# Performance work log

Measured on AMD Instinct MI355X. Metric: run time of the kernel, lower is better.

The kernel has to match this reference:

```python
import jax, jax.numpy as jnp
import numpy as np

EMSIZE = 2048
NCLASS = 128
D1 = 2
D2 = 2
NSENT = 32768


def setup_inputs() -> dict:
    key = jax.random.key(0)
    k1, k2, k3 = jax.random.split(key, 3)
    x = jax.random.normal(k1, (NSENT, 1, EMSIZE), dtype=jnp.float32)
    # Scaled-normal params (original uses nn.init.normal_; scaling keeps tanh unsaturated)
    W1 = jax.random.normal(k2, (D1 + 1, EMSIZE, NCLASS), dtype=jnp.float32) / np.float32(np.sqrt(EMSIZE))
    b1 = jnp.zeros((1, NCLASS), dtype=jnp.float32)
    W2 = jax.random.normal(k3, (D2 + 1, NCLASS, NCLASS), dtype=jnp.float32) / np.float32(np.sqrt(NCLASS))
    b2 = jnp.zeros((1, NCLASS), dtype=jnp.float32)
    return {"structural_representations": x, "W1": W1, "b1": b1, "W2": W2, "b2": b2}


def _shift_down(y, k, n):
    # y[p] -> y[p-k], zeros for p < k (causal shift along sentence axis)
    return jnp.pad(y, ((k, 0), (0, 0)))[:n] if k > 0 else y


def reference(structural_representations, W1, b1, W2, b2):
    x = structural_representations  # [N, 1, E]
    n, _, e = x.shape
    d1 = W1.shape[0] - 1
    d2 = W2.shape[0] - 1
    c = W1.shape[-1]
    xs = x.reshape(n, e)  # [N, E]

    # Stage 1: S[p] = sum_{k=0..d1, k<=p} (x[p-k] @ W1[k] + b1)
    Y = jnp.einsum('ne,kec->knc', xs, W1)  # [d1+1, N, C]: one big GEMM per tap
    S = sum(_shift_down(Y[k], k, n) for k in range(d1 + 1))  # windowed causal sum
    pos = jnp.arange(n)
    cnt1 = (jnp.minimum(pos, d1) + 1).astype(xs.dtype)  # bias added once per valid tap
    H = jnp.tanh(S + cnt1[:, None] * b1[0])  # [N, C]

    # Stage 2 (i >= d2): Z[i] = sum_{j=0..d2} H[i-d2+j] @ W2[j] + (d2+1)*b2
    G = jnp.einsum('nc,kcd->knd', H, W2)  # [d2+1, N, C]
    Z = sum(_shift_down(G[j], d2 - j, n) for j in range(d2 + 1)) + (d2 + 1) * b2[0]

    # Fallback for i < d2: single term tanh(x[i]@W1[0]+b1) @ W2[0] + b2
    H0 = jnp.tanh(xs @ W1[0] + b1[0])
    Z0 = H0 @ W2[0] + b2[0]
    Z = jnp.where((pos >= d2)[:, None], Z, Z0)

    out = jax.nn.log_softmax(Z, axis=-1)
    return out.reshape(n, 1, c)
```

## Files before the change

kernel.cpp:

```cpp
#include <hip/hip_runtime.h>
#include <math.h>

typedef __attribute__((ext_vector_type(8))) short short8;
typedef __attribute__((ext_vector_type(4))) float f32x4;

#define MFMA16(a, b, c) __builtin_amdgcn_mfma_f32_16x16x32_bf16((a), (b), (c), 0, 0, 0)

__device__ inline void gl_lds16(const void* g, void* l) {
  __builtin_amdgcn_global_load_lds(
      (const __attribute__((address_space(1))) void*)g,
      (__attribute__((address_space(3))) void*)l, 16, 0, 0);
}

__device__ inline unsigned int pack2(float lo, float hi) {
  unsigned int ulo = __float_as_uint(lo), uhi = __float_as_uint(hi);
  return (uhi & 0xFFFF0000u) | (ulo >> 16);
}
__device__ inline unsigned short f2bf_r(float f) {
  return (unsigned short)((__float_as_uint(f) + 0x8000u) >> 16);
}
__device__ inline float bf2f(unsigned short h) {
  return __uint_as_float(((unsigned int)h) << 16);
}

__global__ __launch_bounds__(256) void k_repack(const float* __restrict__ W1,
                                                const float* __restrict__ W2,
                                                unsigned short* __restrict__ W1bt,
                                                unsigned short* __restrict__ W2t) {
  __shared__ float tile[64 * 128];
  const int b = blockIdx.x, tid = threadIdx.x;
  if (b < 96) {
    const int k = b >> 5, et = b & 31;
    const int e0 = et * 64;
    const float* src = W1 + (size_t)k * 262144 + (size_t)e0 * 128;
#pragma unroll
    for (int i = 0; i < 8; ++i) {
      int idx4 = tid + i * 256;
      ((f32x4*)tile)[idx4] = ((const f32x4*)src)[idx4];
    }
    __syncthreads();
#pragma unroll
    for (int i = 0; i < 4; ++i) {
      int item = tid + i * 256;
      int c = item >> 3, eo = (item & 7) * 8;
      union { unsigned short h[8]; uint4 v; } t;
#pragma unroll
      for (int u = 0; u < 8; ++u) t.h[u] = f2bf_r(tile[(eo + u) * 128 + c]);
      *(uint4*)(W1bt + (size_t)(k * 128 + c) * 2048 + e0 + eo) = t.v;
    }
  } else {
    int idx = (b - 96) * 256 + tid;
    int j = idx >> 14, r = idx & 16383, d = r >> 7, c = r & 127;
    W2t[idx] = f2bf_r(W2[(size_t)j * 16384 + (size_t)c * 128 + d]);
  }
}

__global__ __launch_bounds__(256, 2) void k_fused(const float* __restrict__ X,
                                                  const unsigned short* __restrict__ Bt,
                                                  const unsigned short* __restrict__ W2t,
                                                  const float* __restrict__ b1,
                                                  const float* __restrict__ b2,
                                                  float* __restrict__ out) {
  __shared__ __align__(16) char smem[66560];
  float* Alds = (float*)smem;
  unsigned short* Blds = (unsigned short*)(smem + 17408);
  unsigned short* Yt = (unsigned short*)smem;
  float* zbuf = (float*)(smem + 62720);

  const int r0 = blockIdx.x * 64;
  const int tid = threadIdx.x, wave = tid >> 6, lane = tid & 63;
  const int mrow = lane & 15, quad = lane >> 4;

  const float* agp[5];
#pragma unroll
  for (int r = 0; r < 4; ++r) {
    int i = wave * 16 + r * 4 + (lane >> 4);
    int g = r0 - 4 + i; if (g < 0) g = 0;
    int c = (lane & 15) ^ (i & 15);
    agp[r] = X + (size_t)g * 2048 + c * 4;
  }
  {
    int i = 64 + (lane >> 4);
    int c = (lane & 15) ^ (i & 15);
    agp[4] = X + (size_t)(r0 - 4 + i) * 2048 + c * 4;
  }
  const unsigned short* bgp[12];
#pragma unroll
  for (int r = 0; r < 12; ++r) {
    int col = wave * 96 + r * 8 + (lane >> 3);
    int c = (lane & 7) ^ (col & 7);
    bgp[r] = Bt + (size_t)col * 2048 + c * 8;
  }

  f32x4 acc[5][6] = {};

  for (int k0 = 0; k0 < 2048; k0 += 64) {
#pragma unroll
    for (int r = 0; r < 4; ++r)
      gl_lds16(agp[r], (char*)Alds + (wave * 16 + r * 4) * 256);
    if (wave == 0) gl_lds16(agp[4], (char*)Alds + 64 * 256);
#pragma unroll
    for (int r = 0; r < 12; ++r)
      gl_lds16(bgp[r], (char*)Blds + (wave * 96 + r * 8) * 128);
#pragma unroll
    for (int r = 0; r < 5; ++r) agp[r] += 64;
#pragma unroll
    for (int r = 0; r < 12; ++r) bgp[r] += 64;
    __syncthreads();

#pragma unroll
    for (int s = 0; s < 2; ++s) {
      short8 af[5];
#pragma unroll
      for (int rt = 0; rt < 5; ++rt) {
        int row = rt * 16 + mrow;
        int c0 = s * 8 + quad * 2;
        const float* base = Alds + row * 64;
        f32x4 x0 = *(const f32x4*)(base + ((c0 ^ mrow) * 4));
        f32x4 x1 = *(const f32x4*)(base + (((c0 + 1) ^ mrow) * 4));
        union { unsigned int u[4]; short8 v; } t;
        t.u[0] = pack2(x0[0], x0[1]); t.u[1] = pack2(x0[2], x0[3]);
        t.u[2] = pack2(x1[0], x1[1]); t.u[3] = pack2(x1[2], x1[3]);
        af[rt] = t.v;
      }
#pragma unroll
      for (int ct = 0; ct < 6; ++ct) {
        int col = wave * 96 + ct * 16 + mrow;
        int ch = (s * 4 + quad) ^ (mrow & 7);
        short8 bf = *(const short8*)(Blds + col * 64 + ch * 8);
#pragma unroll
        for (int rt = 0; rt < 5; ++rt)
          acc[rt][ct] = MFMA16(af[rt], bf, acc[rt][ct]);
      }
    }
    __syncthreads();
  }

#pragma unroll
  for (int rt = 0; rt < 5; ++rt)
#pragma unroll
    for (int ct = 0; ct < 6; ++ct)
#pragma unroll
      for (int rg = 0; rg < 4; ++rg) {
        int l = rt * 16 + quad * 4 + rg;
        int col = wave * 96 + ct * 16 + mrow;
        Yt[l * 392 + col] = f2bf_r(acc[rt][ct][rg]);
      }
  __syncthreads();

  for (int idx = tid; idx < 66 * 128; idx += 256) {
    int hl = idx >> 7, c = idx & 127;
    int p = r0 - 2 + hl;
    int i = hl + 2;
    float h = 0.f;
    if (p >= 0) {
      float s = bf2f(Yt[i * 392 + c]);
      float cnt = 1.f;
      if (p >= 1) { s += bf2f(Yt[(i - 1) * 392 + 128 + c]); cnt += 1.f; }
      if (p >= 2) { s += bf2f(Yt[(i - 2) * 392 + 256 + c]); cnt += 1.f; }
      h = tanhf(fmaf(cnt, b1[c], s));
    }
    Yt[(i - 2) * 392 + 256 + c] = f2bf_r(h);
  }
  __syncthreads();

  f32x4 acc2[8] = {};
#pragma unroll
  for (int j = 0; j < 3; ++j) {
#pragma unroll
    for (int kk = 0; kk < 4; ++kk) {
      short8 a0 = *(const short8*)&Yt[(wave * 16 + mrow + j) * 392 + 256 + kk * 32 + quad * 8];
      const unsigned short* wp = W2t + (size_t)(j * 128 + mrow) * 128 + kk * 32 + quad * 8;
#pragma unroll
      for (int ct = 0; ct < 8; ++ct)
        acc2[ct] = MFMA16(a0, *(const short8*)(wp + ct * 16 * 128), acc2[ct]);
    }
  }

#pragma unroll
  for (int rg = 0; rg < 4; ++rg) {
    float z[8]; float m = -1e30f;
#pragma unroll
    for (int ct = 0; ct < 8; ++ct) {
      z[ct] = acc2[ct][rg] + 3.f * b2[ct * 16 + mrow];
      m = fmaxf(m, z[ct]);
    }
#pragma unroll
    for (int off = 1; off < 16; off <<= 1) m = fmaxf(m, __shfl_xor(m, off, 64));
    float s = 0.f;
#pragma unroll
    for (int ct = 0; ct < 8; ++ct) s += __expf(z[ct] - m);
#pragma unroll
    for (int off = 1; off < 16; off <<= 1) s += __shfl_xor(s, off, 64);
    float lse = m + __logf(s);
    int grow = r0 + wave * 16 + quad * 4 + rg;
    if (grow >= 2) {
      float* op = out + (size_t)grow * 128 + mrow;
#pragma unroll
      for (int ct = 0; ct < 8; ++ct) op[ct * 16] = z[ct] - lse;
    }
  }

  if (blockIdx.x == 0) {
    __syncthreads();
    int row = tid >> 7, d = tid & 127;
    zbuf[row * 128 + d] = tanhf(bf2f(Yt[(row + 4) * 392 + d]) + b1[d]);
    __syncthreads();
    float zv = b2[d];
    for (int c = 0; c < 128; ++c)
      zv = fmaf(zbuf[row * 128 + c], bf2f(W2t[(size_t)d * 128 + c]), zv);
    __syncthreads();
    zbuf[row * 128 + d] = zv;
    __syncthreads();
    float m = -1e30f;
    for (int c = 0; c < 128; ++c) m = fmaxf(m, zbuf[row * 128 + c]);
    float s = 0.f;
    for (int c = 0; c < 128; ++c) s += __expf(zbuf[row * 128 + c] - m);
    out[(size_t)row * 128 + d] = zv - m - __logf(s);
  }
}

extern "C" void kernel_launch(void* const* d_in, const int* in_sizes, int n_in,
                              void* d_out, int out_size, void* d_ws, size_t ws_size,
                              hipStream_t stream) {
  const float* X  = (const float*)d_in[0];
  const float* W1 = (const float*)d_in[1];
  const float* b1 = (const float*)d_in[2];
  const float* W2 = (const float*)d_in[3];
  const float* b2 = (const float*)d_in[4];
  float* out = (float*)d_out;

  unsigned short* W1bt = (unsigned short*)d_ws;
  unsigned short* W2t  = (unsigned short*)((char*)d_ws + 1572864);

  k_repack<<<288, 256, 0, stream>>>(W1, W2, W1bt, W2t);
  k_fused<<<512, 256, 0, stream>>>(X, W1bt, W2t, b1, b2, out);
}
```

Baseline: 424.0 us.

## Double-buffer LDS tiles in fused GEMM main loop, one block per CU

Doubles the shared-memory allocation so the next K-tile of X and W1 can be loaded asynchronously into one buffer while MFMAs read the other. The per-iteration barrier before compute goes away and only the end-of-loop barrier remains. The aim is to hide global-load latency inside each block. In exchange, launch bounds drop to one block per CU, so the 512 blocks now run in two waves and inter-block latency hiding is lost.

```diff
diff --git a/kernel.cpp b/kernel.cpp
--- a/kernel.cpp
+++ b/kernel.cpp
@@ -55,15 +55,13 @@
   }
 }
 
-__global__ __launch_bounds__(256, 2) void k_fused(const float* __restrict__ X,
+__global__ __launch_bounds__(256, 1) void k_fused(const float* __restrict__ X,
                                                   const unsigned short* __restrict__ Bt,
                                                   const unsigned short* __restrict__ W2t,
                                                   const float* __restrict__ b1,
                                                   const float* __restrict__ b2,
                                                   float* __restrict__ out) {
-  __shared__ __align__(16) char smem[66560];
-  float* Alds = (float*)smem;
-  unsigned short* Blds = (unsigned short*)(smem + 17408);
+  __shared__ __align__(16) char smem[133120];
   unsigned short* Yt = (unsigned short*)smem;
   float* zbuf = (float*)(smem + 62720);
 
@@ -94,20 +92,32 @@
 
   f32x4 acc[5][6] = {};
 
-  for (int k0 = 0; k0 < 2048; k0 += 64) {
+  auto stage = [&](char* base) {
+    char* An = base;
+    char* Bn = base + 17408;
 #pragma unroll
     for (int r = 0; r < 4; ++r)
-      gl_lds16(agp[r], (char*)Alds + (wave * 16 + r * 4) * 256);
-    if (wave == 0) gl_lds16(agp[4], (char*)Alds + 64 * 256);
+      gl_lds16(agp[r], An + (wave * 16 + r * 4) * 256);
+    if (wave == 0) gl_lds16(agp[4], An + 64 * 256);
 #pragma unroll
     for (int r = 0; r < 12; ++r)
-      gl_lds16(bgp[r], (char*)Blds + (wave * 96 + r * 8) * 128);
+      gl_lds16(bgp[r], Bn + (wave * 96 + r * 8) * 128);
 #pragma unroll
     for (int r = 0; r < 5; ++r) agp[r] += 64;
 #pragma unroll
     for (int r = 0; r < 12; ++r) bgp[r] += 64;
-    __syncthreads();
-
+  };
+
+  stage(smem);
+  __syncthreads();
+
+#pragma unroll 2
+  for (int t = 0; t < 32; ++t) {
+    const int cur = t & 1;
+    if (t < 31) stage(smem + (cur ^ 1) * 66560);
+
+    const float* Af = (const float*)(smem + cur * 66560);
+    const unsigned short* Bh = (const unsigned short*)(smem + cur * 66560 + 17408);
 #pragma unroll
     for (int s = 0; s < 2; ++s) {
       short8 af[5];
@@ -115,19 +125,19 @@
       for (int rt = 0; rt < 5; ++rt) {
         int row = rt * 16 + mrow;
         int c0 = s * 8 + quad * 2;
-        const float* base = Alds + row * 64;
+        const float* base = Af + row * 64;
         f32x4 x0 = *(const f32x4*)(base + ((c0 ^ mrow) * 4));
         f32x4 x1 = *(const f32x4*)(base + (((c0 + 1) ^ mrow) * 4));
-        union { unsigned int u[4]; short8 v; } t;
-        t.u[0] = pack2(x0[0], x0[1]); t.u[1] = pack2(x0[2], x0[3]);
-        t.u[2] = pack2(x1[0], x1[1]); t.u[3] = pack2(x1[2], x1[3]);
-        af[rt] = t.v;
+        union { unsigned int u[4]; short8 v; } tt;
+        tt.u[0] = pack2(x0[0], x0[1]); tt.u[1] = pack2(x0[2], x0[3]);
+        tt.u[2] = pack2(x1[0], x1[1]); tt.u[3] = pack2(x1[2], x1[3]);
+        af[rt] = tt.v;
       }
 #pragma unroll
       for (int ct = 0; ct < 6; ++ct) {
         int col = wave * 96 + ct * 16 + mrow;
         int ch = (s * 4 + quad) ^ (mrow & 7);
-        short8 bf = *(const short8*)(Blds + col * 64 + ch * 8);
+        short8 bf = *(const short8*)(Bh + col * 64 + ch * 8);
 #pragma unroll
         for (int rt = 0; rt < 5; ++rt)
           acc[rt][ct] = MFMA16(af[rt], bf, acc[rt][ct]);
```

New measurement: 451.9 us. 1.07x slower.

## Prefetch X into registers, convert to bf16 once, double-buffer A in LDS

Applied to the files above, without the earlier changes.

The X tile is no longer staged as fp32 in LDS via direct global-to-LDS loads. Each thread now loads X into registers one iteration ahead with nontemporal loads, packs it to bf16, and writes it into a double-buffered swizzled bf16 LDS tile. The MFMA inner loop then reads bf16 fragments directly instead of converting fp32 to bf16 per wave, which removes redundant conversion and halves A-tile LDS traffic. The change adds manual waitcnt and barrier orchestration, which risks ordering mistakes and extra register pressure under the 2-blocks-per-CU launch bound.

```diff
diff --git a/kernel.cpp b/kernel.cpp
--- a/kernel.cpp
+++ b/kernel.cpp
@@ -62,7 +62,6 @@
                                                   const float* __restrict__ b2,
                                                   float* __restrict__ out) {
   __shared__ __align__(16) char smem[66560];
-  float* Alds = (float*)smem;
   unsigned short* Blds = (unsigned short*)(smem + 17408);
   unsigned short* Yt = (unsigned short*)smem;
   float* zbuf = (float*)(smem + 62720);
@@ -71,19 +70,25 @@
   const int tid = threadIdx.x, wave = tid >> 6, lane = tid & 63;
   const int mrow = lane & 15, quad = lane >> 4;
 
-  const float* agp[5];
-#pragma unroll
-  for (int r = 0; r < 4; ++r) {
-    int i = wave * 16 + r * 4 + (lane >> 4);
-    int g = r0 - 4 + i; if (g < 0) g = 0;
-    int c = (lane & 15) ^ (i & 15);
-    agp[r] = X + (size_t)g * 2048 + c * 4;
-  }
+  const float *ap0, *ap1, *ap2;
+  int lw0, lw1, lw2;
   {
-    int i = 64 + (lane >> 4);
-    int c = (lane & 15) ^ (i & 15);
-    agp[4] = X + (size_t)(r0 - 4 + i) * 2048 + c * 4;
-  }
+    int p, r_, j, g;
+    p = wave * 136 + lane;        r_ = p >> 3; j = p & 7;
+    g = r0 - 4 + r_; if (g < 0) g = 0;
+    ap0 = X + (size_t)g * 2048 + j * 8;
+    lw0 = r_ * 128 + ((j ^ (r_ & 7)) << 4);
+    p += 64;                      r_ = p >> 3; j = p & 7;
+    g = r0 - 4 + r_; if (g < 0) g = 0;
+    ap1 = X + (size_t)g * 2048 + j * 8;
+    lw1 = r_ * 128 + ((j ^ (r_ & 7)) << 4);
+    p += 64;                      r_ = p >> 3; j = p & 7;
+    g = r0 - 4 + r_; if (g < 0) g = 0;
+    ap2 = X + (size_t)g * 2048 + j * 8;
+    lw2 = r_ * 128 + ((j ^ (r_ & 7)) << 4);
+  }
+  f32x4 a0a, a0b, a1a, a1b, a2a, a2b;
+
   const unsigned short* bgp[12];
 #pragma unroll
   for (int r = 0; r < 12; ++r) {
@@ -94,47 +99,77 @@
 
   f32x4 acc[5][6] = {};
 
-  for (int k0 = 0; k0 < 2048; k0 += 64) {
-#pragma unroll
-    for (int r = 0; r < 4; ++r)
-      gl_lds16(agp[r], (char*)Alds + (wave * 16 + r * 4) * 256);
-    if (wave == 0) gl_lds16(agp[4], (char*)Alds + 64 * 256);
+  auto loadA = [&]() {
+    a0a = __builtin_nontemporal_load((const f32x4*)ap0);
+    a0b = __builtin_nontemporal_load((const f32x4*)(ap0 + 4));
+    a1a = __builtin_nontemporal_load((const f32x4*)ap1);
+    a1b = __builtin_nontemporal_load((const f32x4*)(ap1 + 4));
+    if (lane < 8) {
+      a2a = __builtin_nontemporal_load((const f32x4*)ap2);
+      a2b = __builtin_nontemporal_load((const f32x4*)(ap2 + 4));
+    }
+    ap0 += 64; ap1 += 64; ap2 += 64;
+  };
+  auto convA = [&](char* buf) {
+    union { unsigned int u[4]; uint4 v; } t;
+    t.u[0] = pack2(a0a[0], a0a[1]); t.u[1] = pack2(a0a[2], a0a[3]);
+    t.u[2] = pack2(a0b[0], a0b[1]); t.u[3] = pack2(a0b[2], a0b[3]);
+    *(uint4*)(buf + lw0) = t.v;
+    t.u[0] = pack2(a1a[0], a1a[1]); t.u[1] = pack2(a1a[2], a1a[3]);
+    t.u[2] = pack2(a1b[0], a1b[1]); t.u[3] = pack2(a1b[2], a1b[3]);
+    *(uint4*)(buf + lw1) = t.v;
+    if (lane < 8) {
+      t.u[0] = pack2(a2a[0], a2a[1]); t.u[1] = pack2(a2a[2], a2a[3]);
+      t.u[2] = pack2(a2b[0], a2b[1]); t.u[3] = pack2(a2b[2], a2b[3]);
+      *(uint4*)(buf + lw2) = t.v;
+    }
+  };
+  auto stageB = [&]() {
 #pragma unroll
     for (int r = 0; r < 12; ++r)
       gl_lds16(bgp[r], (char*)Blds + (wave * 96 + r * 8) * 128);
 #pragma unroll
-    for (int r = 0; r < 5; ++r) agp[r] += 64;
-#pragma unroll
     for (int r = 0; r < 12; ++r) bgp[r] += 64;
-    __syncthreads();
-
+  };
+  auto compute = [&](const char* buf) {
 #pragma unroll
     for (int s = 0; s < 2; ++s) {
+      const int swz = ((s * 4 + quad) ^ (mrow & 7));
       short8 af[5];
 #pragma unroll
-      for (int rt = 0; rt < 5; ++rt) {
-        int row = rt * 16 + mrow;
-        int c0 = s * 8 + quad * 2;
-        const float* base = Alds + row * 64;
-        f32x4 x0 = *(const f32x4*)(base + ((c0 ^ mrow) * 4));
-        f32x4 x1 = *(const f32x4*)(base + (((c0 + 1) ^ mrow) * 4));
-        union { unsigned int u[4]; short8 v; } t;
-        t.u[0] = pack2(x0[0], x0[1]); t.u[1] = pack2(x0[2], x0[3]);
-        t.u[2] = pack2(x1[0], x1[1]); t.u[3] = pack2(x1[2], x1[3]);
-        af[rt] = t.v;
-      }
+      for (int rt = 0; rt < 5; ++rt)
+        af[rt] = *(const short8*)(buf + (rt * 16 + mrow) * 128 + (swz << 4));
 #pragma unroll
       for (int ct = 0; ct < 6; ++ct) {
         int col = wave * 96 + ct * 16 + mrow;
-        int ch = (s * 4 + quad) ^ (mrow & 7);
-        short8 bf = *(const short8*)(Blds + col * 64 + ch * 8);
+        short8 bf = *(const short8*)(Blds + col * 64 + swz * 8);
 #pragma unroll
         for (int rt = 0; rt < 5; ++rt)
           acc[rt][ct] = MFMA16(af[rt], bf, acc[rt][ct]);
       }
     }
-    __syncthreads();
-  }
+  };
+
+  loadA();
+  convA(smem);
+  loadA();
+  asm volatile("s_waitcnt lgkmcnt(0)" ::: "memory");
+  __builtin_amdgcn_s_barrier();
+  __builtin_amdgcn_sched_barrier(0);
+
+  for (int t = 0; t < 32; ++t) {
+    stageB();
+    if (t < 31) convA(smem + ((t + 1) & 1) * 8704);
+    if (t < 30) loadA();
+    if (t < 30) asm volatile("s_waitcnt vmcnt(6) lgkmcnt(0)" ::: "memory");
+    else        asm volatile("s_waitcnt vmcnt(0) lgkmcnt(0)" ::: "memory");
+    __builtin_amdgcn_s_barrier();
+    __builtin_amdgcn_sched_barrier(0);
+    compute(smem + (t & 1) * 8704);
+    __builtin_amdgcn_s_barrier();
+    __builtin_amdgcn_sched_barrier(0);
+  }
+  __syncthreads();
 
 #pragma unroll
   for (int rt = 0; rt < 5; ++rt)
```

Result: no change. 419.8 us (-1.0%).
